# Kernel optimization log

Hardware: AMD Instinct MI355X
Metric: run time of the kernel (lower is better)

Reference implementation:

```python
import jax, jax.numpy as jnp
import numpy as np

DIM = 256
WIN = 8          # window height == width
HEADS = 8
HEAD_DIM = DIM // HEADS
NW = 64          # number of windows per image
B_IMG = 16
N = WIN * WIN    # 64 tokens per window
B_ = B_IMG * NW  # 1024


def _relative_position_index():
    # matches torch.meshgrid default (ij) indexing
    coords = np.stack(np.meshgrid(np.arange(WIN), np.arange(WIN), indexing='ij'))  # [2,Wh,Ww]
    flat = coords.reshape(2, -1)                                # [2,N]
    rel = flat[:, :, None] - flat[:, None, :]                   # [2,N,N]
    rel = rel.transpose(1, 2, 0).copy()                         # [N,N,2]
    rel[:, :, 0] += WIN - 1
    rel[:, :, 1] += WIN - 1
    rel[:, :, 0] *= 2 * WIN - 1
    return rel.sum(-1).astype(np.int32)                         # [N,N]


def setup_inputs() -> dict:
    key = jax.random.key(0)
    ks = jax.random.split(key, 24)
    std = 0.02

    def lin(i):
        W = jax.random.normal(ks[i], (DIM, DIM), jnp.float32) * std
        b = jax.random.normal(ks[i + 1], (DIM,), jnp.float32) * std
        return W, b

    Wq, bq = lin(0)
    Wk, bk = lin(2)
    Wv, bv = lin(4)
    Wvs, bvs = lin(6)      # v_scale
    Wvh, bvh = lin(8)      # v_shift
    Wpx, bpx = lin(10)     # proj_x
    Wps, bps = lin(12)     # proj_scale
    Wph, bph = lin(14)     # proj_shift

    bias_table = jax.random.normal(ks[16], ((2 * WIN - 1) * (2 * WIN - 1), HEADS), jnp.float32) * std
    rel_idx = jnp.asarray(_relative_position_index())

    q_input = jax.random.normal(ks[17], (B_, N, DIM), jnp.float32)
    k_input = jax.random.normal(ks[18], (B_, N, DIM), jnp.float32)
    v_input = jax.random.normal(ks[19], (B_, N, DIM), jnp.float32)
    scale_in = jax.random.normal(ks[20], (B_, N, DIM), jnp.float32)
    shift_in = jax.random.normal(ks[21], (B_, N, DIM), jnp.float32)

    # shifted-window style mask: 0 where attendable, large negative otherwise
    u = jax.random.uniform(ks[22], (NW, N, N), jnp.float32)
    mask = jnp.where(u < 0.15, -100.0, 0.0).astype(jnp.float32)

    return {
        'q_input': q_input, 'k_input': k_input, 'v_input': v_input,
        'scale_in': scale_in, 'shift_in': shift_in, 'mask': mask,
        'Wq': Wq, 'bq': bq, 'Wk': Wk, 'bk': bk, 'Wv': Wv, 'bv': bv,
        'Wvs': Wvs, 'bvs': bvs, 'Wvh': Wvh, 'bvh': bvh,
        'Wpx': Wpx, 'bpx': bpx, 'Wps': Wps, 'bps': bps, 'Wph': Wph, 'bph': bph,
        'bias_table': bias_table, 'rel_idx': rel_idx,
    }


def reference(q_input, k_input, v_input, scale_in, shift_in, mask,
              Wq, bq, Wk, bk, Wv, bv, Wvs, bvs, Wvh, bvh,
              Wpx, bpx, Wps, bps, Wph, bph, bias_table, rel_idx):
    B, Ntok, C = q_input.shape
    scale = HEAD_DIM ** -0.5

    def to_heads(x, W, b):
        # nn.Linear: x @ W.T + b, then split heads -> [B, H, N, hd]
        return (x @ W.T + b).reshape(B, Ntok, HEADS, HEAD_DIM).transpose(0, 2, 1, 3)

    q = to_heads(q_input, Wq, bq) * scale
    k = to_heads(k_input, Wk, bk)
    v = to_heads(v_input, Wv, bv)
    v_scale = to_heads(scale_in, Wvs, bvs)
    v_shift = to_heads(shift_in, Wvh, bvh)

    attn = jnp.einsum('bhnd,bhmd->bhnm', q, k)                    # [B,H,N,N]
    rel_bias = bias_table[rel_idx]                                # [N,N,H] gather
    attn = attn + rel_bias.transpose(2, 0, 1)[None]               # add per-head bias

    nW = mask.shape[0]
    attn = attn.reshape(B // nW, nW, HEADS, Ntok, Ntok) + mask[None, :, None]
    attn = jax.nn.softmax(attn.reshape(B, HEADS, Ntok, Ntok), axis=-1)

    def out_proj(val, Wp, bp):
        o = jnp.einsum('bhnm,bhmd->bhnd', attn, val)
        o = o.transpose(0, 2, 1, 3).reshape(B, Ntok, C)
        return o @ Wp.T + bp

    x_out = out_proj(v, Wpx, bpx)
    scale_out = out_proj(v_scale, Wps, bps)
    shift_out = out_proj(v_shift, Wph, bph)
    return (x_out, scale_out, shift_out)
```

## Files before the change

kernel.cpp:

```cpp
#include <hip/hip_runtime.h>


typedef __attribute__((ext_vector_type(8))) __bf16 bf16x8;
typedef __attribute__((ext_vector_type(4))) float f32x4;
typedef __attribute__((ext_vector_type(4))) unsigned short u16x4;

#define LOFF_QS 16384
#define LOFF_KS 32768
#define LOFF_PS 49152

__device__ __forceinline__ unsigned short f2bf(float f) {
  unsigned int u = __float_as_uint(f);
  u += 0x7FFFu + ((u >> 16) & 1u);
  return (unsigned short)(u >> 16);
}

__device__ __forceinline__ int swz256(int row, int col) {
  return row * 256 + (col ^ ((row & 31) << 3));
}
__device__ __forceinline__ int swz64(int row, int col) {
  return row * 64 + (col ^ ((row & 7) << 3));
}

__global__ void pack_weights(const float* __restrict__ W0, const float* __restrict__ W1,
                             const float* __restrict__ W2, const float* __restrict__ W3,
                             const float* __restrict__ W4, const float* __restrict__ W5,
                             const float* __restrict__ W6, const float* __restrict__ W7,
                             unsigned short* __restrict__ pk) {
  int t = blockIdx.x * 256 + threadIdx.x;
  int wsel = t >> 13;
  int rem  = t & 8191;
  int cb   = rem >> 9;
  int kc   = (rem >> 6) & 7;
  int l    = rem & 63;
  const float* W = (wsel == 0) ? W0 : (wsel == 1) ? W1 : (wsel == 2) ? W2 : (wsel == 3) ? W3
                 : (wsel == 4) ? W4 : (wsel == 5) ? W5 : (wsel == 6) ? W6 : W7;
  int row = cb * 16 + (l & 15);
  int col = kc * 32 + ((l >> 4) << 3);
  const float* src = W + row * 256 + col;
  unsigned short* dst = pk + (size_t)t * 8;
#pragma unroll
  for (int i = 0; i < 8; ++i) dst[i] = f2bf(src[i]);
}

__global__ void make_bm(const float* __restrict__ mask, const float* __restrict__ btab,
                        const int* __restrict__ ridx, float* __restrict__ bm) {
  int t = blockIdx.x * 256 + threadIdx.x;
  int j = t & 63;
  int i = (t >> 6) & 63;
  int h = (t >> 12) & 7;
  int wi = t >> 15;
  bm[t] = mask[(wi * 64 + i) * 64 + j] + btab[ridx[i * 64 + j] * 8 + h];
}

__device__ __forceinline__ void stage_x(unsigned short* XS, const float* __restrict__ X,
                                        int b, int tid) {
  const float4* src = reinterpret_cast<const float4*>(X + (size_t)b * 16384);
#pragma unroll
  for (int it = 0; it < 8; ++it) {
    int f = it * 512 + tid;
    float4 v = src[f];
    int row = f >> 6;
    int col = (f & 63) << 2;
    u16x4 p;
    p[0] = f2bf(v.x); p[1] = f2bf(v.y); p[2] = f2bf(v.z); p[3] = f2bf(v.w);
    *reinterpret_cast<u16x4*>(XS + swz256(row, col)) = p;
  }
}

__device__ __forceinline__ void proj_core(const unsigned short* __restrict__ aTile,
                                          const unsigned short* __restrict__ pw,
                                          const float* __restrict__ bias, float scale,
                                          int lane, int w, f32x4 acc[4][2]) {
  const int r16 = lane & 15, c4 = lane >> 4;
  f32x4 z = {0.f, 0.f, 0.f, 0.f};
#pragma unroll
  for (int mf = 0; mf < 4; ++mf)
#pragma unroll
    for (int nf = 0; nf < 2; ++nf) acc[mf][nf] = z;
#pragma unroll
  for (int kc = 0; kc < 8; ++kc) {
    bf16x8 a[4];
#pragma unroll
    for (int mf = 0; mf < 4; ++mf) {
      int row = mf * 16 + r16;
      int col = kc * 32 + (c4 << 3);
      a[mf] = *reinterpret_cast<const bf16x8*>(aTile + swz256(row, col));
    }
    bf16x8 bb[2];
#pragma unroll
    for (int nf = 0; nf < 2; ++nf)
      bb[nf] = *reinterpret_cast<const bf16x8*>(pw + ((((2 * w + nf) * 8 + kc) * 64 + lane) << 3));
#pragma unroll
    for (int mf = 0; mf < 4; ++mf)
#pragma unroll
      for (int nf = 0; nf < 2; ++nf)
        acc[mf][nf] = __builtin_amdgcn_mfma_f32_16x16x32_bf16(a[mf], bb[nf], acc[mf][nf], 0, 0, 0);
  }
  float b0 = bias[w * 32 + r16];
  float b1 = bias[w * 32 + 16 + r16];
#pragma unroll
  for (int mf = 0; mf < 4; ++mf)
#pragma unroll
    for (int r = 0; r < 4; ++r) {
      acc[mf][0][r] = (acc[mf][0][r] + b0) * scale;
      acc[mf][1][r] = (acc[mf][1][r] + b1) * scale;
    }
}

__device__ __forceinline__ void store_rm_bf16(unsigned short* dst, const f32x4 acc[4][2],
                                              int lane, int w) {
  const int r16 = lane & 15, c4 = lane >> 4;
#pragma unroll
  for (int mf = 0; mf < 4; ++mf)
#pragma unroll
    for (int nf = 0; nf < 2; ++nf)
#pragma unroll
      for (int r = 0; r < 4; ++r) {
        int row = mf * 16 + c4 * 4 + r;
        int col = w * 32 + nf * 16 + r16;
        dst[swz256(row, col)] = f2bf(acc[mf][nf][r]);
      }
}

__device__ __forceinline__ void store_tr_bf16(unsigned short* dst, const f32x4 acc[4][2],
                                              int lane, int w) {
  const int r16 = lane & 15, c4 = lane >> 4;
#pragma unroll
  for (int mf = 0; mf < 4; ++mf)
#pragma unroll
    for (int nf = 0; nf < 2; ++nf)
#pragma unroll
      for (int r = 0; r < 4; ++r) {
        int vrow = w * 32 + nf * 16 + r16;
        int vcol = mf * 16 + c4 * 4 + r;
        dst[swz64(vrow, vcol)] = f2bf(acc[mf][nf][r]);
      }
}

__device__ __forceinline__ void store_gl_f32(float* __restrict__ dst, const f32x4 acc[4][2],
                                             int lane, int w) {
  const int r16 = lane & 15, c4 = lane >> 4;
#pragma unroll
  for (int mf = 0; mf < 4; ++mf)
#pragma unroll
    for (int nf = 0; nf < 2; ++nf)
#pragma unroll
      for (int r = 0; r < 4; ++r) {
        int row = mf * 16 + c4 * 4 + r;
        int col = w * 32 + nf * 16 + r16;
        dst[row * 256 + col] = acc[mf][nf][r];
      }
}

__device__ __forceinline__ void attn_core(const unsigned short* __restrict__ sm,
                                          const float* __restrict__ bmw,
                                          int lane, int w, unsigned short* Ps) {
  const int r16 = lane & 15, c4 = lane >> 4;
  const unsigned short* Qs = sm + LOFF_QS;
  const unsigned short* Ks = sm + LOFF_KS;
  bf16x8 aq[4], bk4[4];
#pragma unroll
  for (int mf = 0; mf < 4; ++mf)
    aq[mf] = *reinterpret_cast<const bf16x8*>(Qs + swz256(mf * 16 + r16, w * 32 + (c4 << 3)));
#pragma unroll
  for (int nf = 0; nf < 4; ++nf)
    bk4[nf] = *reinterpret_cast<const bf16x8*>(Ks + swz256(nf * 16 + r16, w * 32 + (c4 << 3)));
  f32x4 z = {0.f, 0.f, 0.f, 0.f};
  f32x4 s[4][4];
#pragma unroll
  for (int mf = 0; mf < 4; ++mf)
#pragma unroll
    for (int nf = 0; nf < 4; ++nf)
      s[mf][nf] = __builtin_amdgcn_mfma_f32_16x16x32_bf16(aq[mf], bk4[nf], z, 0, 0, 0);
#pragma unroll
  for (int mf = 0; mf < 4; ++mf)
#pragma unroll
    for (int r = 0; r < 4; ++r) {
      int row = mf * 16 + c4 * 4 + r;
      const float* bp = bmw + row * 64 + r16;
      float v0 = s[mf][0][r] + bp[0];
      float v1 = s[mf][1][r] + bp[16];
      float v2 = s[mf][2][r] + bp[32];
      float v3 = s[mf][3][r] + bp[48];
      float m = fmaxf(fmaxf(v0, v1), fmaxf(v2, v3));
      m = fmaxf(m, __shfl_xor(m, 1));
      m = fmaxf(m, __shfl_xor(m, 2));
      m = fmaxf(m, __shfl_xor(m, 4));
      m = fmaxf(m, __shfl_xor(m, 8));
      float e0 = __expf(v0 - m), e1 = __expf(v1 - m);
      float e2 = __expf(v2 - m), e3 = __expf(v3 - m);
      float sum = e0 + e1 + e2 + e3;
      sum += __shfl_xor(sum, 1);
      sum += __shfl_xor(sum, 2);
      sum += __shfl_xor(sum, 4);
      sum += __shfl_xor(sum, 8);
      float inv = 1.0f / sum;
      Ps[swz64(row, r16)]      = f2bf(e0 * inv);
      Ps[swz64(row, r16 + 16)] = f2bf(e1 * inv);
      Ps[swz64(row, r16 + 32)] = f2bf(e2 * inv);
      Ps[swz64(row, r16 + 48)] = f2bf(e3 * inv);
    }
}

__device__ __forceinline__ void pv_core(const unsigned short* __restrict__ Ps,
                                        const unsigned short* __restrict__ Vt,
                                        int lane, int w, f32x4 o[4][2]) {
  const int r16 = lane & 15, c4 = lane >> 4;
  f32x4 z = {0.f, 0.f, 0.f, 0.f};
#pragma unroll
  for (int mf = 0; mf < 4; ++mf)
#pragma unroll
    for (int nf = 0; nf < 2; ++nf) o[mf][nf] = z;
#pragma unroll
  for (int kc = 0; kc < 2; ++kc) {
    bf16x8 a[4];
#pragma unroll
    for (int mf = 0; mf < 4; ++mf)
      a[mf] = *reinterpret_cast<const bf16x8*>(Ps + swz64(mf * 16 + r16, kc * 32 + (c4 << 3)));
    bf16x8 bb[2];
#pragma unroll
    for (int nf = 0; nf < 2; ++nf)
      bb[nf] = *reinterpret_cast<const bf16x8*>(Vt + swz64(w * 32 + nf * 16 + r16, kc * 32 + (c4 << 3)));
#pragma unroll
    for (int mf = 0; mf < 4; ++mf)
#pragma unroll
      for (int nf = 0; nf < 2; ++nf)
        o[mf][nf] = __builtin_amdgcn_mfma_f32_16x16x32_bf16(a[mf], bb[nf], o[mf][nf], 0, 0, 0);
  }
}

__global__ __launch_bounds__(512, 2) void win_attn(
    const float* __restrict__ gq, const float* __restrict__ gk, const float* __restrict__ gv,
    const float* __restrict__ gsc, const float* __restrict__ gsh,
    const unsigned short* __restrict__ pk,
    const float* __restrict__ b_q, const float* __restrict__ b_k, const float* __restrict__ b_v,
    const float* __restrict__ b_vs, const float* __restrict__ b_vh,
    const float* __restrict__ b_px, const float* __restrict__ b_ps, const float* __restrict__ b_ph,
    const float* __restrict__ bm, float* __restrict__ out) {
  __shared__ __align__(16) unsigned short sm[81920];
  const int b    = blockIdx.x;
  const int tid  = threadIdx.x;
  const int lane = tid & 63;
  const int w    = tid >> 6;

  unsigned short* XS = sm;
  unsigned short* QS = sm + LOFF_QS;
  unsigned short* KS = sm + LOFF_KS;
  unsigned short* PS = sm + LOFF_PS + w * 4096;

  f32x4 acc[4][2];

  stage_x(XS, gq, b, tid);
  __syncthreads();
  proj_core(XS, pk, b_q, 0.17677669529663687f, lane, w, acc);
  store_rm_bf16(QS, acc, lane, w);
  __syncthreads();
  stage_x(XS, gk, b, tid);
  __syncthreads();
  proj_core(XS, pk + 65536, b_k, 1.0f, lane, w, acc);
  store_rm_bf16(KS, acc, lane, w);
  __syncthreads();
  stage_x(XS, gv, b, tid);
  attn_core(sm, bm + (size_t)(((b & 63) * 8 + w) << 12), lane, w, PS);
  __syncthreads();
  proj_core(XS, pk + 2 * 65536, b_v, 1.0f, lane, w, acc);
  store_tr_bf16(QS, acc, lane, w);
  __syncthreads();
  stage_x(XS, gsc, b, tid);
  {
    f32x4 o[4][2];
    pv_core(PS, QS, lane, w, o);
    store_rm_bf16(KS, o, lane, w);
  }
  __syncthreads();
  proj_core(KS, pk + 5 * 65536, b_px, 1.0f, lane, w, acc);
  store_gl_f32(out + (size_t)b * 16384, acc, lane, w);
  proj_core(XS, pk + 3 * 65536, b_vs, 1.0f, lane, w, acc);
  store_tr_bf16(QS, acc, lane, w);
  __syncthreads();
  stage_x(XS, gsh, b, tid);
  {
    f32x4 o[4][2];
    pv_core(PS, QS, lane, w, o);
    store_rm_bf16(KS, o, lane, w);
  }
  __syncthreads();
  proj_core(KS, pk + 6 * 65536, b_ps, 1.0f, lane, w, acc);
  store_gl_f32(out + 16777216 + (size_t)b * 16384, acc, lane, w);
  proj_core(XS, pk + 4 * 65536, b_vh, 1.0f, lane, w, acc);
  store_tr_bf16(QS, acc, lane, w);
  __syncthreads();
  {
    f32x4 o[4][2];
    pv_core(PS, QS, lane, w, o);
    store_rm_bf16(KS, o, lane, w);
  }
  __syncthreads();
  proj_core(KS, pk + 7 * 65536, b_ph, 1.0f, lane, w, acc);
  store_gl_f32(out + 33554432 + (size_t)b * 16384, acc, lane, w);
}

extern "C" void kernel_launch(void* const* d_in, const int* in_sizes, int n_in,
                              void* d_out, int out_size, void* d_ws, size_t ws_size,
                              hipStream_t stream) {
  const float* Xq   = (const float*)d_in[0];
  const float* Xk   = (const float*)d_in[1];
  const float* Xv   = (const float*)d_in[2];
  const float* Xsc  = (const float*)d_in[3];
  const float* Xsh  = (const float*)d_in[4];
  const float* mask = (const float*)d_in[5];
  const float* Wq   = (const float*)d_in[6];  const float* bq  = (const float*)d_in[7];
  const float* Wk   = (const float*)d_in[8];  const float* bk  = (const float*)d_in[9];
  const float* Wv   = (const float*)d_in[10]; const float* bv  = (const float*)d_in[11];
  const float* Wvs  = (const float*)d_in[12]; const float* bvs = (const float*)d_in[13];
  const float* Wvh  = (const float*)d_in[14]; const float* bvh = (const float*)d_in[15];
  const float* Wpx  = (const float*)d_in[16]; const float* bpx = (const float*)d_in[17];
  const float* Wps  = (const float*)d_in[18]; const float* bps = (const float*)d_in[19];
  const float* Wph  = (const float*)d_in[20]; const float* bph = (const float*)d_in[21];
  const float* btab = (const float*)d_in[22];
  const int*   ridx = (const int*)d_in[23];

  unsigned short* pk = (unsigned short*)d_ws;
  float* bm = (float*)((char*)d_ws + (size_t)8 * 65536 * 2);

  pack_weights<<<256, 256, 0, stream>>>(Wq, Wk, Wv, Wvs, Wvh, Wpx, Wps, Wph, pk);
  make_bm<<<8192, 256, 0, stream>>>(mask, btab, ridx, bm);
  win_attn<<<1024, 512, 0, stream>>>(Xq, Xk, Xv, Xsc, Xsh, pk,
                                     bq, bk, bv, bvs, bvh, bpx, bps, bph,
                                     bm, (float*)d_out);
}
```

Measured before the change: 215.3 us.

## Rewrite window attention to keep Q/K/P/V fragments in registers with 4 waves

The fused kernel now runs with 256 threads per block. Each wave owns 64 output columns (two heads), and Q, K, P and V are kept as MFMA fragments in registers. Accumulator layouts are converted with lane shuffles ('butterfly') rather than round-tripped through LDS, which shrinks shared memory from 160KB to 64KB. Global loads of the next input are software-pipelined into registers while the current projection runs. The bias+mask table is pre-permuted into the fragment layout for vectorized loads, and bf16 conversion uses the native cast. The aim is fewer LDS round-trips and barriers, at the cost of heavy register pressure that may spill at 2 blocks per CU.

```diff
diff --git a/kernel.cpp b/kernel.cpp
--- a/kernel.cpp
+++ b/kernel.cpp
@@ -5,21 +5,17 @@
 typedef __attribute__((ext_vector_type(4))) float f32x4;
 typedef __attribute__((ext_vector_type(4))) unsigned short u16x4;
 
-#define LOFF_QS 16384
-#define LOFF_KS 32768
-#define LOFF_PS 49152
-
 __device__ __forceinline__ unsigned short f2bf(float f) {
-  unsigned int u = __float_as_uint(f);
-  u += 0x7FFFu + ((u >> 16) & 1u);
-  return (unsigned short)(u >> 16);
-}
-
+  return __builtin_bit_cast(unsigned short, (__bf16)f);
+}
+__device__ __forceinline__ unsigned pk2(float lo, float hi) {
+  return (unsigned)f2bf(lo) | ((unsigned)f2bf(hi) << 16);
+}
 __device__ __forceinline__ int swz256(int row, int col) {
   return row * 256 + (col ^ ((row & 31) << 3));
 }
-__device__ __forceinline__ int swz64(int row, int col) {
-  return row * 64 + (col ^ ((row & 7) << 3));
+__device__ __forceinline__ f32x4 mfma16(bf16x8 a, bf16x8 b, f32x4 c) {
+  return __builtin_amdgcn_mfma_f32_16x16x32_bf16(a, b, c, 0, 0, 0);
 }
 
 __global__ void pack_weights(const float* __restrict__ W0, const float* __restrict__ W1,
@@ -28,277 +24,374 @@
                              const float* __restrict__ W6, const float* __restrict__ W7,
                              unsigned short* __restrict__ pk) {
   int t = blockIdx.x * 256 + threadIdx.x;
-  int wsel = t >> 13;
-  int rem  = t & 8191;
-  int cb   = rem >> 9;
-  int kc   = (rem >> 6) & 7;
-  int l    = rem & 63;
-  const float* W = (wsel == 0) ? W0 : (wsel == 1) ? W1 : (wsel == 2) ? W2 : (wsel == 3) ? W3
-                 : (wsel == 4) ? W4 : (wsel == 5) ? W5 : (wsel == 6) ? W6 : W7;
-  int row = cb * 16 + (l & 15);
-  int col = kc * 32 + ((l >> 4) << 3);
-  const float* src = W + row * 256 + col;
+  int mat = t >> 13;
+  int w   = (t >> 11) & 3;
+  int blk = (t >> 9) & 3;
+  int kc  = (t >> 6) & 7;
+  int l   = t & 63;
+  const float* W = (mat == 0) ? W0 : (mat == 1) ? W1 : (mat == 2) ? W2 : (mat == 3) ? W3
+                 : (mat == 4) ? W4 : (mat == 5) ? W5 : (mat == 6) ? W6 : W7;
+  const float* src = W + (64 * w + 16 * blk + (l & 15)) * 256 + 32 * kc + 8 * (l >> 4);
   unsigned short* dst = pk + (size_t)t * 8;
 #pragma unroll
   for (int i = 0; i < 8; ++i) dst[i] = f2bf(src[i]);
 }
 
-__global__ void make_bm(const float* __restrict__ mask, const float* __restrict__ btab,
-                        const int* __restrict__ ridx, float* __restrict__ bm) {
+__global__ void make_bmt(const float* __restrict__ mask, const float* __restrict__ btab,
+                         const int* __restrict__ ridx, float* __restrict__ bmt) {
   int t = blockIdx.x * 256 + threadIdx.x;
-  int j = t & 63;
-  int i = (t >> 6) & 63;
-  int h = (t >> 12) & 7;
+  int r  = t & 3;
+  int l  = (t >> 2) & 63;
+  int mf = (t >> 8) & 3;
+  int nf = (t >> 10) & 3;
+  int h  = (t >> 12) & 7;
   int wi = t >> 15;
-  bm[t] = mask[(wi * 64 + i) * 64 + j] + btab[ridx[i * 64 + j] * 8 + h];
-}
-
-__device__ __forceinline__ void stage_x(unsigned short* XS, const float* __restrict__ X,
-                                        int b, int tid) {
-  const float4* src = reinterpret_cast<const float4*>(X + (size_t)b * 16384);
+  int q = 16 * nf + (l & 15);
+  int k = 16 * mf + 4 * (l >> 4) + r;
+  bmt[t] = mask[(wi * 64 + q) * 64 + k] + btab[ridx[q * 64 + k] * 8 + h];
+}
+
+__device__ __forceinline__ bf16x8 butterfly(f32x4 C0, f32x4 C1, int c4, int r16) {
+  unsigned a0 = pk2(C0[0], C0[1]), a1 = pk2(C0[2], C0[3]);
+  unsigned b0 = pk2(C1[0], C1[1]), b1 = pk2(C1[2], C1[3]);
+  int src0 = (((2 * c4) & 3) << 4) + r16;
+  int src1 = (((2 * c4 + 1) & 3) << 4) + r16;
+  unsigned A0 = (unsigned)__shfl((int)a0, src0);
+  unsigned A1 = (unsigned)__shfl((int)a1, src0);
+  unsigned A2 = (unsigned)__shfl((int)a0, src1);
+  unsigned A3 = (unsigned)__shfl((int)a1, src1);
+  unsigned B0 = (unsigned)__shfl((int)b0, src0);
+  unsigned B1 = (unsigned)__shfl((int)b1, src0);
+  unsigned B2 = (unsigned)__shfl((int)b0, src1);
+  unsigned B3 = (unsigned)__shfl((int)b1, src1);
+  bool hi = c4 >= 2;
+  union { unsigned u[4]; bf16x8 v; } r;
+  r.u[0] = hi ? B0 : A0;
+  r.u[1] = hi ? B1 : A1;
+  r.u[2] = hi ? B2 : A2;
+  r.u[3] = hi ? B3 : A3;
+  return r.v;
+}
+
+__device__ __forceinline__ void load8(f32x4 r[8], const float* __restrict__ X,
+                                      int b, int tid, int half) {
+  const f32x4* src = reinterpret_cast<const f32x4*>(X + (size_t)b * 16384) + half * 2048;
+#pragma unroll
+  for (int it = 0; it < 8; ++it) r[it] = src[it * 256 + tid];
+}
+__device__ __forceinline__ void write8(unsigned short* T, const f32x4 r[8], int tid, int half) {
 #pragma unroll
   for (int it = 0; it < 8; ++it) {
-    int f = it * 512 + tid;
-    float4 v = src[f];
+    int f = half * 2048 + it * 256 + tid;
     int row = f >> 6;
     int col = (f & 63) << 2;
     u16x4 p;
-    p[0] = f2bf(v.x); p[1] = f2bf(v.y); p[2] = f2bf(v.z); p[3] = f2bf(v.w);
-    *reinterpret_cast<u16x4*>(XS + swz256(row, col)) = p;
-  }
-}
-
-__device__ __forceinline__ void proj_core(const unsigned short* __restrict__ aTile,
-                                          const unsigned short* __restrict__ pw,
-                                          const float* __restrict__ bias, float scale,
-                                          int lane, int w, f32x4 acc[4][2]) {
+    p[0] = f2bf(r[it][0]); p[1] = f2bf(r[it][1]);
+    p[2] = f2bf(r[it][2]); p[3] = f2bf(r[it][3]);
+    *reinterpret_cast<u16x4*>(T + swz256(row, col)) = p;
+  }
+}
+
+__device__ __forceinline__ void projT(const unsigned short* __restrict__ T,
+                                      const unsigned short* __restrict__ pw,
+                                      const float* __restrict__ bias, float scale,
+                                      int lane, int w, bf16x8 frag[2][4]) {
   const int r16 = lane & 15, c4 = lane >> 4;
   f32x4 z = {0.f, 0.f, 0.f, 0.f};
+  f32x4 acc[4][4];
 #pragma unroll
   for (int mf = 0; mf < 4; ++mf)
 #pragma unroll
-    for (int nf = 0; nf < 2; ++nf) acc[mf][nf] = z;
+    for (int nf = 0; nf < 4; ++nf) acc[mf][nf] = z;
 #pragma unroll
   for (int kc = 0; kc < 8; ++kc) {
-    bf16x8 a[4];
-#pragma unroll
-    for (int mf = 0; mf < 4; ++mf) {
-      int row = mf * 16 + r16;
-      int col = kc * 32 + (c4 << 3);
-      a[mf] = *reinterpret_cast<const bf16x8*>(aTile + swz256(row, col));
-    }
-    bf16x8 bb[2];
-#pragma unroll
-    for (int nf = 0; nf < 2; ++nf)
-      bb[nf] = *reinterpret_cast<const bf16x8*>(pw + ((((2 * w + nf) * 8 + kc) * 64 + lane) << 3));
-#pragma unroll
-    for (int mf = 0; mf < 4; ++mf)
-#pragma unroll
-      for (int nf = 0; nf < 2; ++nf)
-        acc[mf][nf] = __builtin_amdgcn_mfma_f32_16x16x32_bf16(a[mf], bb[nf], acc[mf][nf], 0, 0, 0);
-  }
-  float b0 = bias[w * 32 + r16];
-  float b1 = bias[w * 32 + 16 + r16];
-#pragma unroll
-  for (int mf = 0; mf < 4; ++mf)
-#pragma unroll
-    for (int r = 0; r < 4; ++r) {
-      acc[mf][0][r] = (acc[mf][0][r] + b0) * scale;
-      acc[mf][1][r] = (acc[mf][1][r] + b1) * scale;
-    }
-}
-
-__device__ __forceinline__ void store_rm_bf16(unsigned short* dst, const f32x4 acc[4][2],
-                                              int lane, int w) {
-  const int r16 = lane & 15, c4 = lane >> 4;
-#pragma unroll
-  for (int mf = 0; mf < 4; ++mf)
-#pragma unroll
-    for (int nf = 0; nf < 2; ++nf)
-#pragma unroll
-      for (int r = 0; r < 4; ++r) {
-        int row = mf * 16 + c4 * 4 + r;
-        int col = w * 32 + nf * 16 + r16;
-        dst[swz256(row, col)] = f2bf(acc[mf][nf][r]);
-      }
-}
-
-__device__ __forceinline__ void store_tr_bf16(unsigned short* dst, const f32x4 acc[4][2],
-                                              int lane, int w) {
-  const int r16 = lane & 15, c4 = lane >> 4;
-#pragma unroll
-  for (int mf = 0; mf < 4; ++mf)
-#pragma unroll
-    for (int nf = 0; nf < 2; ++nf)
-#pragma unroll
-      for (int r = 0; r < 4; ++r) {
-        int vrow = w * 32 + nf * 16 + r16;
-        int vcol = mf * 16 + c4 * 4 + r;
-        dst[swz64(vrow, vcol)] = f2bf(acc[mf][nf][r]);
-      }
-}
-
-__device__ __forceinline__ void store_gl_f32(float* __restrict__ dst, const f32x4 acc[4][2],
-                                             int lane, int w) {
-  const int r16 = lane & 15, c4 = lane >> 4;
-#pragma unroll
-  for (int mf = 0; mf < 4; ++mf)
-#pragma unroll
-    for (int nf = 0; nf < 2; ++nf)
-#pragma unroll
-      for (int r = 0; r < 4; ++r) {
-        int row = mf * 16 + c4 * 4 + r;
-        int col = w * 32 + nf * 16 + r16;
-        dst[row * 256 + col] = acc[mf][nf][r];
-      }
-}
-
-__device__ __forceinline__ void attn_core(const unsigned short* __restrict__ sm,
-                                          const float* __restrict__ bmw,
-                                          int lane, int w, unsigned short* Ps) {
-  const int r16 = lane & 15, c4 = lane >> 4;
-  const unsigned short* Qs = sm + LOFF_QS;
-  const unsigned short* Ks = sm + LOFF_KS;
-  bf16x8 aq[4], bk4[4];
-#pragma unroll
-  for (int mf = 0; mf < 4; ++mf)
-    aq[mf] = *reinterpret_cast<const bf16x8*>(Qs + swz256(mf * 16 + r16, w * 32 + (c4 << 3)));
-#pragma unroll
-  for (int nf = 0; nf < 4; ++nf)
-    bk4[nf] = *reinterpret_cast<const bf16x8*>(Ks + swz256(nf * 16 + r16, w * 32 + (c4 << 3)));
-  f32x4 z = {0.f, 0.f, 0.f, 0.f};
-  f32x4 s[4][4];
-#pragma unroll
-  for (int mf = 0; mf < 4; ++mf)
-#pragma unroll
-    for (int nf = 0; nf < 4; ++nf)
-      s[mf][nf] = __builtin_amdgcn_mfma_f32_16x16x32_bf16(aq[mf], bk4[nf], z, 0, 0, 0);
-#pragma unroll
-  for (int mf = 0; mf < 4; ++mf)
-#pragma unroll
-    for (int r = 0; r < 4; ++r) {
-      int row = mf * 16 + c4 * 4 + r;
-      const float* bp = bmw + row * 64 + r16;
-      float v0 = s[mf][0][r] + bp[0];
-      float v1 = s[mf][1][r] + bp[16];
-      float v2 = s[mf][2][r] + bp[32];
-      float v3 = s[mf][3][r] + bp[48];
-      float m = fmaxf(fmaxf(v0, v1), fmaxf(v2, v3));
-      m = fmaxf(m, __shfl_xor(m, 1));
-      m = fmaxf(m, __shfl_xor(m, 2));
-      m = fmaxf(m, __shfl_xor(m, 4));
-      m = fmaxf(m, __shfl_xor(m, 8));
-      float e0 = __expf(v0 - m), e1 = __expf(v1 - m);
-      float e2 = __expf(v2 - m), e3 = __expf(v3 - m);
-      float sum = e0 + e1 + e2 + e3;
-      sum += __shfl_xor(sum, 1);
-      sum += __shfl_xor(sum, 2);
-      sum += __shfl_xor(sum, 4);
-      sum += __shfl_xor(sum, 8);
-      float inv = 1.0f / sum;
-      Ps[swz64(row, r16)]      = f2bf(e0 * inv);
-      Ps[swz64(row, r16 + 16)] = f2bf(e1 * inv);
-      Ps[swz64(row, r16 + 32)] = f2bf(e2 * inv);
-      Ps[swz64(row, r16 + 48)] = f2bf(e3 * inv);
-    }
-}
-
-__device__ __forceinline__ void pv_core(const unsigned short* __restrict__ Ps,
-                                        const unsigned short* __restrict__ Vt,
-                                        int lane, int w, f32x4 o[4][2]) {
+    bf16x8 aw[4], bx[4];
+#pragma unroll
+    for (int mf = 0; mf < 4; ++mf)
+      aw[mf] = *reinterpret_cast<const bf16x8*>(pw + (((mf * 8 + kc) * 64 + lane) << 3));
+#pragma unroll
+    for (int nf = 0; nf < 4; ++nf)
+      bx[nf] = *reinterpret_cast<const bf16x8*>(T + swz256(16 * nf + r16, 32 * kc + 8 * c4));
+#pragma unroll
+    for (int mf = 0; mf < 4; ++mf)
+#pragma unroll
+      for (int nf = 0; nf < 4; ++nf) acc[mf][nf] = mfma16(aw[mf], bx[nf], acc[mf][nf]);
+  }
+#pragma unroll
+  for (int mf = 0; mf < 4; ++mf) {
+    f32x4 b4 = *reinterpret_cast<const f32x4*>(bias + 64 * w + 16 * mf + 4 * c4);
+#pragma unroll
+    for (int nf = 0; nf < 4; ++nf)
+#pragma unroll
+      for (int r = 0; r < 4; ++r) acc[mf][nf][r] = (acc[mf][nf][r] + b4[r]) * scale;
+  }
+#pragma unroll
+  for (int bp = 0; bp < 2; ++bp)
+#pragma unroll
+    for (int nf = 0; nf < 4; ++nf)
+      frag[bp][nf] = butterfly(acc[2 * bp][nf], acc[2 * bp + 1][nf], c4, r16);
+}
+
+__device__ __forceinline__ void projN(const unsigned short* __restrict__ T,
+                                      const unsigned short* __restrict__ pw,
+                                      int lane, f32x4 acc[4][4]) {
   const int r16 = lane & 15, c4 = lane >> 4;
   f32x4 z = {0.f, 0.f, 0.f, 0.f};
 #pragma unroll
   for (int mf = 0; mf < 4; ++mf)
 #pragma unroll
-    for (int nf = 0; nf < 2; ++nf) o[mf][nf] = z;
-#pragma unroll
-  for (int kc = 0; kc < 2; ++kc) {
-    bf16x8 a[4];
-#pragma unroll
-    for (int mf = 0; mf < 4; ++mf)
-      a[mf] = *reinterpret_cast<const bf16x8*>(Ps + swz64(mf * 16 + r16, kc * 32 + (c4 << 3)));
-    bf16x8 bb[2];
-#pragma unroll
-    for (int nf = 0; nf < 2; ++nf)
-      bb[nf] = *reinterpret_cast<const bf16x8*>(Vt + swz64(w * 32 + nf * 16 + r16, kc * 32 + (c4 << 3)));
-#pragma unroll
-    for (int mf = 0; mf < 4; ++mf)
-#pragma unroll
-      for (int nf = 0; nf < 2; ++nf)
-        o[mf][nf] = __builtin_amdgcn_mfma_f32_16x16x32_bf16(a[mf], bb[nf], o[mf][nf], 0, 0, 0);
-  }
-}
-
-__global__ __launch_bounds__(512, 2) void win_attn(
+    for (int nf = 0; nf < 4; ++nf) acc[mf][nf] = z;
+#pragma unroll
+  for (int kc = 0; kc < 8; ++kc) {
+    bf16x8 a[4], bb[4];
+#pragma unroll
+    for (int mf = 0; mf < 4; ++mf)
+      a[mf] = *reinterpret_cast<const bf16x8*>(T + swz256(16 * mf + r16, 32 * kc + 8 * c4));
+#pragma unroll
+    for (int nf = 0; nf < 4; ++nf)
+      bb[nf] = *reinterpret_cast<const bf16x8*>(pw + (((nf * 8 + kc) * 64 + lane) << 3));
+#pragma unroll
+    for (int mf = 0; mf < 4; ++mf)
+#pragma unroll
+      for (int nf = 0; nf < 4; ++nf) acc[mf][nf] = mfma16(a[mf], bb[nf], acc[mf][nf]);
+  }
+}
+
+__device__ __forceinline__ void vEpilogue(f32x4 acc[4][4], const float* __restrict__ bias,
+                                          int lane, int w, bf16x8 Vf[4][2]) {
+  const int r16 = lane & 15, c4 = lane >> 4;
+#pragma unroll
+  for (int nf = 0; nf < 4; ++nf) {
+    float bb = bias[64 * w + 16 * nf + r16];
+#pragma unroll
+    for (int mf = 0; mf < 4; ++mf)
+#pragma unroll
+      for (int r = 0; r < 4; ++r) acc[mf][nf][r] += bb;
+  }
+#pragma unroll
+  for (int bp = 0; bp < 2; ++bp)
+#pragma unroll
+    for (int nf = 0; nf < 4; ++nf)
+      Vf[nf][bp] = butterfly(acc[2 * bp][nf], acc[2 * bp + 1][nf], c4, r16);
+}
+
+__device__ __forceinline__ void storeOut(float* __restrict__ dst, f32x4 acc[4][4],
+                                         const float* __restrict__ bias, int lane, int w) {
+  const int r16 = lane & 15, c4 = lane >> 4;
+#pragma unroll
+  for (int nf = 0; nf < 4; ++nf) {
+    float bb = bias[64 * w + 16 * nf + r16];
+#pragma unroll
+    for (int mf = 0; mf < 4; ++mf)
+#pragma unroll
+      for (int r = 0; r < 4; ++r)
+        dst[(16 * mf + 4 * c4 + r) * 256 + 64 * w + 16 * nf + r16] = acc[mf][nf][r] + bb;
+  }
+}
+
+__device__ __forceinline__ void storeO(unsigned short* T, const f32x4 o[2][4],
+                                       int hh, int lane, int w) {
+  const int r16 = lane & 15, c4 = lane >> 4;
+#pragma unroll
+  for (int mfd = 0; mfd < 2; ++mfd)
+#pragma unroll
+    for (int nf = 0; nf < 4; ++nf)
+#pragma unroll
+      for (int r = 0; r < 4; ++r)
+        T[swz256(16 * nf + r16, 64 * w + 32 * hh + 16 * mfd + 4 * c4 + r)] =
+            f2bf(o[mfd][nf][r]);
+}
+
+__global__ __launch_bounds__(256, 2) void win_attn(
     const float* __restrict__ gq, const float* __restrict__ gk, const float* __restrict__ gv,
     const float* __restrict__ gsc, const float* __restrict__ gsh,
     const unsigned short* __restrict__ pk,
     const float* __restrict__ b_q, const float* __restrict__ b_k, const float* __restrict__ b_v,
     const float* __restrict__ b_vs, const float* __restrict__ b_vh,
     const float* __restrict__ b_px, const float* __restrict__ b_ps, const float* __restrict__ b_ph,
-    const float* __restrict__ bm, float* __restrict__ out) {
-  __shared__ __align__(16) unsigned short sm[81920];
+    const float* __restrict__ bmt, float* __restrict__ out) {
+  __shared__ __align__(16) unsigned short sm[32768];
+  unsigned short* R0 = sm;
+  unsigned short* R1 = sm + 16384;
+
   const int b    = blockIdx.x;
   const int tid  = threadIdx.x;
   const int lane = tid & 63;
   const int w    = tid >> 6;
-
-  unsigned short* XS = sm;
-  unsigned short* QS = sm + LOFF_QS;
-  unsigned short* KS = sm + LOFF_KS;
-  unsigned short* PS = sm + LOFF_PS + w * 4096;
-
-  f32x4 acc[4][2];
-
-  stage_x(XS, gq, b, tid);
-  __syncthreads();
-  proj_core(XS, pk, b_q, 0.17677669529663687f, lane, w, acc);
-  store_rm_bf16(QS, acc, lane, w);
-  __syncthreads();
-  stage_x(XS, gk, b, tid);
-  __syncthreads();
-  proj_core(XS, pk + 65536, b_k, 1.0f, lane, w, acc);
-  store_rm_bf16(KS, acc, lane, w);
-  __syncthreads();
-  stage_x(XS, gv, b, tid);
-  attn_core(sm, bm + (size_t)(((b & 63) * 8 + w) << 12), lane, w, PS);
-  __syncthreads();
-  proj_core(XS, pk + 2 * 65536, b_v, 1.0f, lane, w, acc);
-  store_tr_bf16(QS, acc, lane, w);
-  __syncthreads();
-  stage_x(XS, gsc, b, tid);
-  {
-    f32x4 o[4][2];
-    pv_core(PS, QS, lane, w, o);
-    store_rm_bf16(KS, o, lane, w);
-  }
-  __syncthreads();
-  proj_core(KS, pk + 5 * 65536, b_px, 1.0f, lane, w, acc);
-  store_gl_f32(out + (size_t)b * 16384, acc, lane, w);
-  proj_core(XS, pk + 3 * 65536, b_vs, 1.0f, lane, w, acc);
-  store_tr_bf16(QS, acc, lane, w);
-  __syncthreads();
-  stage_x(XS, gsh, b, tid);
-  {
-    f32x4 o[4][2];
-    pv_core(PS, QS, lane, w, o);
-    store_rm_bf16(KS, o, lane, w);
-  }
-  __syncthreads();
-  proj_core(KS, pk + 6 * 65536, b_ps, 1.0f, lane, w, acc);
-  store_gl_f32(out + 16777216 + (size_t)b * 16384, acc, lane, w);
-  proj_core(XS, pk + 4 * 65536, b_vh, 1.0f, lane, w, acc);
-  store_tr_bf16(QS, acc, lane, w);
-  __syncthreads();
-  {
-    f32x4 o[4][2];
-    pv_core(PS, QS, lane, w, o);
-    store_rm_bf16(KS, o, lane, w);
-  }
-  __syncthreads();
-  proj_core(KS, pk + 7 * 65536, b_ph, 1.0f, lane, w, acc);
-  store_gl_f32(out + 33554432 + (size_t)b * 16384, acc, lane, w);
+  const int r16  = lane & 15, c4 = lane >> 4;
+  const int wi   = b & 63;
+
+  f32x4 rSa[8], rSb[8];
+  f32x4 z = {0.f, 0.f, 0.f, 0.f};
+
+  load8(rSa, gq, b, tid, 0);
+  load8(rSb, gq, b, tid, 1);
+  write8(R0, rSa, tid, 0);
+  write8(R0, rSb, tid, 1);
+  __syncthreads();
+
+  bf16x8 Qf[2][4], Kf[2][4], Pf[2][2][4];
+
+  load8(rSa, gk, b, tid, 0);
+  load8(rSb, gk, b, tid, 1);
+  projT(R0, pk + (size_t)(0 * 4 + w) * 16384, b_q, 0.17677669529663687f, lane, w, Qf);
+  write8(R1, rSa, tid, 0);
+  write8(R1, rSb, tid, 1);
+  __syncthreads();
+
+  load8(rSa, gv, b, tid, 0);
+  load8(rSb, gv, b, tid, 1);
+  projT(R1, pk + (size_t)(1 * 4 + w) * 16384, b_k, 1.0f, lane, w, Kf);
+  write8(R0, rSa, tid, 0);
+  write8(R0, rSb, tid, 1);
+  __syncthreads();
+
+#pragma unroll
+  for (int hh = 0; hh < 2; ++hh) {
+    if (hh == 0) load8(rSa, gsc, b, tid, 0);
+    else         load8(rSb, gsc, b, tid, 1);
+    const float* bmb = bmt + ((size_t)(wi * 8 + 2 * w + hh) << 12);
+#pragma unroll
+    for (int nf = 0; nf < 4; ++nf) {
+      f32x4 s[4];
+#pragma unroll
+      for (int mf = 0; mf < 4; ++mf) s[mf] = mfma16(Kf[hh][mf], Qf[hh][nf], z);
+      float e[4][4];
+      float mx = -1e30f;
+#pragma unroll
+      for (int mf = 0; mf < 4; ++mf) {
+        f32x4 bm4 = *reinterpret_cast<const f32x4*>(bmb + (((nf * 4 + mf) * 64 + lane) << 2));
+#pragma unroll
+        for (int r = 0; r < 4; ++r) {
+          float vv = s[mf][r] + bm4[r];
+          e[mf][r] = vv;
+          mx = fmaxf(mx, vv);
+        }
+      }
+      mx = fmaxf(mx, __shfl_xor(mx, 16));
+      mx = fmaxf(mx, __shfl_xor(mx, 32));
+      float sum = 0.f;
+#pragma unroll
+      for (int mf = 0; mf < 4; ++mf)
+#pragma unroll
+        for (int r = 0; r < 4; ++r) {
+          float ev = __expf(e[mf][r] - mx);
+          e[mf][r] = ev;
+          sum += ev;
+        }
+      sum += __shfl_xor(sum, 16);
+      sum += __shfl_xor(sum, 32);
+      float inv = 1.0f / sum;
+#pragma unroll
+      for (int kc = 0; kc < 2; ++kc) {
+        f32x4 p0, p1;
+#pragma unroll
+        for (int r = 0; r < 4; ++r) {
+          p0[r] = e[2 * kc][r] * inv;
+          p1[r] = e[2 * kc + 1][r] * inv;
+        }
+        Pf[hh][kc][nf] = butterfly(p0, p1, c4, r16);
+      }
+    }
+    if (hh == 0) write8(R1, rSa, tid, 0);
+    else         write8(R1, rSb, tid, 1);
+  }
+  __syncthreads();
+
+  bf16x8 Vf[4][2];
+  f32x4 o0[2][4], o1[2][4];
+
+  {
+    f32x4 vacc[4][4];
+    projN(R0, pk + (size_t)(2 * 4 + w) * 16384, lane, vacc);
+    vEpilogue(vacc, b_v, lane, w, Vf);
+  }
+#pragma unroll
+  for (int mfd = 0; mfd < 2; ++mfd)
+#pragma unroll
+    for (int nf = 0; nf < 4; ++nf) { o0[mfd][nf] = z; o1[mfd][nf] = z; }
+#pragma unroll
+  for (int kc = 0; kc < 2; ++kc)
+#pragma unroll
+    for (int mfd = 0; mfd < 2; ++mfd)
+#pragma unroll
+      for (int nf = 0; nf < 4; ++nf) {
+        o0[mfd][nf] = mfma16(Vf[0 + mfd][kc], Pf[0][kc][nf], o0[mfd][nf]);
+        o1[mfd][nf] = mfma16(Vf[2 + mfd][kc], Pf[1][kc][nf], o1[mfd][nf]);
+      }
+  __syncthreads();
+  storeO(R0, o0, 0, lane, w);
+  storeO(R0, o1, 1, lane, w);
+  __syncthreads();
+
+  load8(rSa, gsh, b, tid, 0);
+  {
+    f32x4 acc[4][4];
+    projN(R0, pk + (size_t)(5 * 4 + w) * 16384, lane, acc);
+    storeOut(out + (size_t)b * 16384, acc, b_px, lane, w);
+  }
+
+  {
+    f32x4 vacc[4][4];
+    projN(R1, pk + (size_t)(3 * 4 + w) * 16384, lane, vacc);
+    vEpilogue(vacc, b_vs, lane, w, Vf);
+  }
+#pragma unroll
+  for (int mfd = 0; mfd < 2; ++mfd)
+#pragma unroll
+    for (int nf = 0; nf < 4; ++nf) { o0[mfd][nf] = z; o1[mfd][nf] = z; }
+#pragma unroll
+  for (int kc = 0; kc < 2; ++kc)
+#pragma unroll
+    for (int mfd = 0; mfd < 2; ++mfd)
+#pragma unroll
+      for (int nf = 0; nf < 4; ++nf) {
+        o0[mfd][nf] = mfma16(Vf[0 + mfd][kc], Pf[0][kc][nf], o0[mfd][nf]);
+        o1[mfd][nf] = mfma16(Vf[2 + mfd][kc], Pf[1][kc][nf], o1[mfd][nf]);
+      }
+  __syncthreads();
+  storeO(R1, o0, 0, lane, w);
+  storeO(R1, o1, 1, lane, w);
+  __syncthreads();
+
+  write8(R0, rSa, tid, 0);
+  load8(rSb, gsh, b, tid, 1);
+  {
+    f32x4 acc[4][4];
+    projN(R1, pk + (size_t)(6 * 4 + w) * 16384, lane, acc);
+    storeOut(out + 16777216 + (size_t)b * 16384, acc, b_ps, lane, w);
+  }
+  write8(R0, rSb, tid, 1);
+  __syncthreads();
+
+  {
+    f32x4 vacc[4][4];
+    projN(R0, pk + (size_t)(4 * 4 + w) * 16384, lane, vacc);
+    vEpilogue(vacc, b_vh, lane, w, Vf);
+  }
+#pragma unroll
+  for (int mfd = 0; mfd < 2; ++mfd)
+#pragma unroll
+    for (int nf = 0; nf < 4; ++nf) { o0[mfd][nf] = z; o1[mfd][nf] = z; }
+#pragma unroll
+  for (int kc = 0; kc < 2; ++kc)
+#pragma unroll
+    for (int mfd = 0; mfd < 2; ++mfd)
+#pragma unroll
+      for (int nf = 0; nf < 4; ++nf) {
+        o0[mfd][nf] = mfma16(Vf[0 + mfd][kc], Pf[0][kc][nf], o0[mfd][nf]);
+        o1[mfd][nf] = mfma16(Vf[2 + mfd][kc], Pf[1][kc][nf], o1[mfd][nf]);
+      }
+  __syncthreads();
+  storeO(R0, o0, 0, lane, w);
+  storeO(R0, o1, 1, lane, w);
+  __syncthreads();
+
+  {
+    f32x4 acc[4][4];
+    projN(R0, pk + (size_t)(7 * 4 + w) * 16384, lane, acc);
+    storeOut(out + 33554432 + (size_t)b * 16384, acc, b_ph, lane, w);
+  }
 }
 
 extern "C" void kernel_launch(void* const* d_in, const int* in_sizes, int n_in,
@@ -322,11 +415,11 @@
   const int*   ridx = (const int*)d_in[23];
 
   unsigned short* pk = (unsigned short*)d_ws;
-  float* bm = (float*)((char*)d_ws + (size_t)8 * 65536 * 2);
+  float* bmt = (float*)((char*)d_ws + (size_t)8 * 65536 * 2);
 
   pack_weights<<<256, 256, 0, stream>>>(Wq, Wk, Wv, Wvs, Wvh, Wpx, Wps, Wph, pk);
-  make_bm<<<8192, 256, 0, stream>>>(mask, btab, ridx, bm);
-  win_attn<<<1024, 512, 0, stream>>>(Xq, Xk, Xv, Xsc, Xsh, pk,
+  make_bmt<<<8192, 256, 0, stream>>>(mask, btab, ridx, bmt);
+  win_attn<<<1024, 256, 0, stream>>>(Xq, Xk, Xv, Xsc, Xsh, pk,
                                      bq, bk, bv, bvs, bvh, bpx, bps, bph,
-                                     bm, (float*)d_out);
-}
+                                     bmt, (float*)d_out);
+}
```

Result: slower. 365.5 us (+69.8%).
